# Performance work log

Hardware: AMD Instinct MI355X
Metric: run time of the kernel (lower is better)

## Reference

```python
import jax, jax.numpy as jnp
import numpy as np

D_MODEL = 2048
D_STATE = 16
KER = 4
DT_RANK = D_MODEL // 16  # mamba default: ceil(d_model/16) = 128
B_SZ = 2
SEQ = 1024


def setup_inputs() -> dict:
    key = jax.random.key(0)
    ks = jax.random.split(key, 8)
    s = 0.02
    return {
        "x": jax.random.normal(ks[0], (B_SZ, SEQ, D_MODEL), jnp.float32),
        # in_proj: d_model -> 2*d_inner (expand=1 so d_inner=d_model)
        "W_in": jax.random.normal(ks[1], (2 * D_MODEL, D_MODEL), jnp.float32) * s,
        # depthwise causal conv, one kernel of length KER per channel
        "conv_w": jax.random.normal(ks[2], (D_MODEL, KER), jnp.float32) * s,
        "conv_b": jnp.zeros((D_MODEL,), jnp.float32),
        # x_proj: d_inner -> dt_rank + 2*d_state
        "W_xproj": jax.random.normal(ks[3], (DT_RANK + 2 * D_STATE, D_MODEL), jnp.float32) * s,
        # dt_proj: dt_rank -> d_inner
        "W_dt": jax.random.normal(ks[4], (D_MODEL, DT_RANK), jnp.float32) * s,
        "b_dt": jax.random.uniform(ks[5], (D_MODEL,), jnp.float32, -4.0, -2.0),
        # S4D-real init: A = -[1..d_state] per channel, stored as log
        "A_log": jnp.log(jnp.broadcast_to(jnp.arange(1, D_STATE + 1, dtype=jnp.float32), (D_MODEL, D_STATE))),
        "Dskip": jnp.ones((D_MODEL,), jnp.float32),
        # out_proj: d_inner -> d_model
        "W_out": jax.random.normal(ks[6], (D_MODEL, D_MODEL), jnp.float32) * s,
    }


def _mamba(x, W_in, conv_w, conv_b, W_xproj, W_dt, b_dt, A_log, Dskip, W_out):
    Bsz, L, dm = x.shape
    d_state = A_log.shape[1]
    dt_rank = W_dt.shape[1]
    K = conv_w.shape[1]

    # in_proj -> gate z and ssm input u
    xz = x @ W_in.T                      # [B, L, 2*d_inner]
    u, z = jnp.split(xz, 2, axis=-1)     # each [B, L, d_inner]

    # causal depthwise conv1d over time, then SiLU
    up = jnp.pad(u, ((0, 0), (K - 1, 0), (0, 0)))
    conv = conv_b + sum(conv_w[:, k] * up[:, k:k + L, :] for k in range(K))
    u = jax.nn.silu(conv)                # [B, L, d_inner]

    # input-dependent dt, B, C
    x_dbl = u @ W_xproj.T                # [B, L, dt_rank + 2*d_state]
    dt_r = x_dbl[..., :dt_rank]
    Bm = x_dbl[..., dt_rank:dt_rank + d_state]      # [B, L, N]
    Cm = x_dbl[..., dt_rank + d_state:]             # [B, L, N]
    dt = jax.nn.softplus(dt_r @ W_dt.T + b_dt)      # [B, L, d_inner]

    A = -jnp.exp(A_log)                             # [d_inner, N]
    dA = jnp.exp(dt[..., None] * A)                 # [B, L, d_inner, N]
    dBu = dt[..., None] * Bm[:, :, None, :] * u[..., None]  # [B, L, d_inner, N]

    def step(h, inp):
        dA_t, dBu_t, C_t = inp
        h = dA_t * h + dBu_t                        # [B, d_inner, N]
        y_t = jnp.einsum('bdn,bn->bd', h, C_t)      # [B, d_inner]
        return h, y_t

    h0 = jnp.zeros((Bsz, dm, d_state), dtype=x.dtype)
    _, ys = jax.lax.scan(step, h0,
                         (dA.swapaxes(0, 1), dBu.swapaxes(0, 1), Cm.swapaxes(0, 1)))
    y = ys.swapaxes(0, 1) + u * Dskip               # [B, L, d_inner]
    y = y * jax.nn.silu(z)
    return y @ W_out.T                              # [B, L, d_model]


def reference(x, W_in, conv_w, conv_b, W_xproj, W_dt, b_dt, A_log, Dskip, W_out):
    return _mamba(x, W_in, conv_w, conv_b, W_xproj, W_dt, b_dt, A_log, Dskip, W_out)
```

## Files before the change

### kernel.cpp

```cpp
#include <hip/hip_runtime.h>
#include <hip/hip_bf16.h>


#define D_MODEL 2048
#define D_STATE 16
#define KER 4
#define DT_RANK 128
#define B_SZ 2
#define SEQ 1024
#define BL (B_SZ * SEQ)
#define XPROJ_N (DT_RANK + 2 * D_STATE)
#define NC 32
#define TC (SEQ / NC)

using f32x4  = __attribute__((ext_vector_type(4))) float;
using bf16x8 = __attribute__((ext_vector_type(8))) __bf16;
using bf16x4 = __attribute__((ext_vector_type(4))) __bf16;

__device__ __forceinline__ float softplusf(float x) {
    return (x > 20.f) ? x : log1pf(__expf(x));
}
__device__ __forceinline__ float siluf(float x) {
    return x / (1.f + __expf(-x));
}

__device__ __forceinline__ void split4(const float* __restrict__ src,
                                       __bf16* __restrict__ hi,
                                       __bf16* __restrict__ lo, int i) {
    float4 v = *reinterpret_cast<const float4*>(&src[(size_t)i * 4]);
    bf16x4 hv, lv;
    float f[4] = {v.x, v.y, v.z, v.w};
    #pragma unroll
    for (int j = 0; j < 4; ++j) {
        __bf16 h = (__bf16)f[j];
        hv[j] = h;
        lv[j] = (__bf16)(f[j] - (float)h);
    }
    *reinterpret_cast<bf16x4*>(&hi[(size_t)i * 4]) = hv;
    *reinterpret_cast<bf16x4*>(&lo[(size_t)i * 4]) = lv;
}

__global__ __launch_bounds__(256) void split_all_kernel(
    const float* __restrict__ x,  __bf16* __restrict__ xh,  __bf16* __restrict__ xl,
    const float* __restrict__ wi, __bf16* __restrict__ wih, __bf16* __restrict__ wil,
    const float* __restrict__ wo, __bf16* __restrict__ woh, __bf16* __restrict__ wol,
    const float* __restrict__ wd, __bf16* __restrict__ wdh, __bf16* __restrict__ wdl)
{
    const int NX = BL * D_MODEL / 4;
    const int NI = 2 * D_MODEL * D_MODEL / 4;
    const int NO = D_MODEL * D_MODEL / 4;
    const int ND = D_MODEL * DT_RANK / 4;
    const int total = NX + NI + NO + ND;
    for (int i = blockIdx.x * 256 + threadIdx.x; i < total; i += gridDim.x * 256) {
        if      (i < NX)           split4(x,  xh,  xl,  i);
        else if (i < NX + NI)      split4(wi, wih, wil, i - NX);
        else if (i < NX + NI + NO) split4(wo, woh, wol, i - NX - NI);
        else                       split4(wd, wdh, wdl, i - NX - NI - NO);
    }
}

template <int EPI>
__global__ __launch_bounds__(256, 2) void gemm_bf3(
    const __bf16* __restrict__ Ah, const __bf16* __restrict__ Al,
    const __bf16* __restrict__ Wh, const __bf16* __restrict__ Wl,
    float* __restrict__ C, const float* __restrict__ bias, int N_, int K)
{
    __shared__ __align__(16) __bf16 lds[4 * 128 * 64];
    __bf16* sAh = lds;
    __bf16* sAl = lds + 8192;
    __bf16* sWh = lds + 16384;
    __bf16* sWl = lds + 24576;

    const int tid = threadIdx.x;
    const int bm = blockIdx.y * 128;
    const int bn = blockIdx.x * 128;
    const int w  = tid >> 6;
    const int l  = tid & 63;
    const int wr = (w >> 1) * 64;
    const int wc = (w & 1) * 64;
    const int fr = l & 15;
    const int fq = l >> 4;

    f32x4 acc[4][4] = {};

    for (int k0 = 0; k0 < K; k0 += 64) {
        #pragma unroll
        for (int i = 0; i < 4; ++i) {
            const int f  = i * 256 + tid;
            const int r  = f >> 3;
            const int ss = f & 7;
            const int gs = ss ^ (r & 7);
            const size_t ga = (size_t)(bm + r) * K + k0 + gs * 8;
            const size_t gw = (size_t)(bn + r) * K + k0 + gs * 8;
            __builtin_amdgcn_global_load_lds(
                (const __attribute__((address_space(1))) void*)(Ah + ga),
                (__attribute__((address_space(3))) void*)(sAh + (size_t)f * 8), 16, 0, 0);
            __builtin_amdgcn_global_load_lds(
                (const __attribute__((address_space(1))) void*)(Al + ga),
                (__attribute__((address_space(3))) void*)(sAl + (size_t)f * 8), 16, 0, 0);
            __builtin_amdgcn_global_load_lds(
                (const __attribute__((address_space(1))) void*)(Wh + gw),
                (__attribute__((address_space(3))) void*)(sWh + (size_t)f * 8), 16, 0, 0);
            __builtin_amdgcn_global_load_lds(
                (const __attribute__((address_space(1))) void*)(Wl + gw),
                (__attribute__((address_space(3))) void*)(sWl + (size_t)f * 8), 16, 0, 0);
        }
        __syncthreads();

        #pragma unroll
        for (int ks = 0; ks < 2; ++ks) {
            bf16x8 ah[4], al[4], wh[4], wl[4];
            #pragma unroll
            for (int t = 0; t < 4; ++t) {
                const int ra = wr + t * 16 + fr;
                const int sa = (ks * 4 + fq) ^ (ra & 7);
                ah[t] = *reinterpret_cast<const bf16x8*>(&sAh[ra * 64 + sa * 8]);
                al[t] = *reinterpret_cast<const bf16x8*>(&sAl[ra * 64 + sa * 8]);
                const int rw = wc + t * 16 + fr;
                const int sw = (ks * 4 + fq) ^ (rw & 7);
                wh[t] = *reinterpret_cast<const bf16x8*>(&sWh[rw * 64 + sw * 8]);
                wl[t] = *reinterpret_cast<const bf16x8*>(&sWl[rw * 64 + sw * 8]);
            }
            #pragma unroll
            for (int mt = 0; mt < 4; ++mt)
                #pragma unroll
                for (int nt = 0; nt < 4; ++nt) {
                    acc[mt][nt] = __builtin_amdgcn_mfma_f32_16x16x32_bf16(
                        ah[mt], wh[nt], acc[mt][nt], 0, 0, 0);
                    acc[mt][nt] = __builtin_amdgcn_mfma_f32_16x16x32_bf16(
                        ah[mt], wl[nt], acc[mt][nt], 0, 0, 0);
                    acc[mt][nt] = __builtin_amdgcn_mfma_f32_16x16x32_bf16(
                        al[mt], wh[nt], acc[mt][nt], 0, 0, 0);
                }
        }
        __syncthreads();
    }

    #pragma unroll
    for (int mt = 0; mt < 4; ++mt)
        #pragma unroll
        for (int nt = 0; nt < 4; ++nt) {
            const int gn = bn + wc + nt * 16 + fr;
            #pragma unroll
            for (int j = 0; j < 4; ++j) {
                float v = acc[mt][nt][j];
                if (EPI == 1) v = softplusf(v + bias[gn]);
                C[(size_t)(bm + wr + mt * 16 + fq * 4 + j) * N_ + gn] = v;
            }
        }
}

#define BKT 32
#define XBM 64
#define XBN 32
#define XKS 8
#define XKC (D_MODEL / XKS)

__global__ __launch_bounds__(256) void xdbl_partial(
    const float* __restrict__ A,
    const float* __restrict__ W,
    float* __restrict__ P)
{
    __shared__ float As[BKT][XBM + 4];
    __shared__ float Ws[BKT][XBN + 4];

    const int tid = threadIdx.x;
    const int bm = blockIdx.y * XBM;
    const int bn = blockIdx.x * XBN;
    const int ks = blockIdx.z;
    const int tx = tid & 7;
    const int ty = tid >> 3;

    float acc[2][4] = {};

    const int kend = (ks + 1) * XKC;
    for (int k0 = ks * XKC; k0 < kend; k0 += BKT) {
        #pragma unroll
        for (int i = 0; i < 2; ++i) {
            int f = tid + i * 256;
            int row = f >> 3;
            int kq  = f & 7;
            float4 v = *reinterpret_cast<const float4*>(
                &A[(size_t)(bm + row) * D_MODEL + k0 + kq * 4]);
            As[kq * 4 + 0][row] = v.x;
            As[kq * 4 + 1][row] = v.y;
            As[kq * 4 + 2][row] = v.z;
            As[kq * 4 + 3][row] = v.w;
        }
        {
            int row = tid >> 3;
            int kq  = tid & 7;
            float4 v = *reinterpret_cast<const float4*>(
                &W[(size_t)(bn + row) * D_MODEL + k0 + kq * 4]);
            Ws[kq * 4 + 0][row] = v.x;
            Ws[kq * 4 + 1][row] = v.y;
            Ws[kq * 4 + 2][row] = v.z;
            Ws[kq * 4 + 3][row] = v.w;
        }
        __syncthreads();

        #pragma unroll
        for (int kk = 0; kk < BKT; ++kk) {
            float a0 = As[kk][ty * 2 + 0];
            float a1 = As[kk][ty * 2 + 1];
            float4 w4 = *reinterpret_cast<const float4*>(&Ws[kk][tx * 4]);
            float wv[4] = {w4.x, w4.y, w4.z, w4.w};
            #pragma unroll
            for (int j = 0; j < 4; ++j) {
                acc[0][j] = fmaf(a0, wv[j], acc[0][j]);
                acc[1][j] = fmaf(a1, wv[j], acc[1][j]);
            }
        }
        __syncthreads();
    }

    #pragma unroll
    for (int i = 0; i < 2; ++i) {
        const int gm = bm + ty * 2 + i;
        #pragma unroll
        for (int j = 0; j < 4; ++j) {
            const int gn = bn + tx * 4 + j;
            P[((size_t)ks * BL + gm) * XPROJ_N + gn] = acc[i][j];
        }
    }
}

__global__ __launch_bounds__(256) void xdbl_reduce(
    const float* __restrict__ P, float* __restrict__ xdbl,
    __bf16* __restrict__ xdh, __bf16* __restrict__ xdl)
{
    const int i = blockIdx.x * 256 + threadIdx.x;
    const int n4 = BL * XPROJ_N / 4;
    if (i >= n4) return;
    float4 s = *reinterpret_cast<const float4*>(&P[(size_t)i * 4]);
    #pragma unroll
    for (int ks = 1; ks < XKS; ++ks) {
        float4 v = *reinterpret_cast<const float4*>(
            &P[(size_t)ks * BL * XPROJ_N + (size_t)i * 4]);
        s.x += v.x; s.y += v.y; s.z += v.z; s.w += v.w;
    }
    *reinterpret_cast<float4*>(&xdbl[(size_t)i * 4]) = s;

    const int row = i / (XPROJ_N / 4);
    const int col = (i % (XPROJ_N / 4)) * 4;
    if (col < DT_RANK) {
        bf16x4 hv, lv;
        float f[4] = {s.x, s.y, s.z, s.w};
        #pragma unroll
        for (int j = 0; j < 4; ++j) {
            __bf16 h = (__bf16)f[j];
            hv[j] = h;
            lv[j] = (__bf16)(f[j] - (float)h);
        }
        *reinterpret_cast<bf16x4*>(&xdh[(size_t)row * DT_RANK + col]) = hv;
        *reinterpret_cast<bf16x4*>(&xdl[(size_t)row * DT_RANK + col]) = lv;
    }
}

__global__ __launch_bounds__(256) void conv_silu_kernel(
    const float* __restrict__ xz,
    const float* __restrict__ conv_w,
    const float* __restrict__ conv_b,
    float* __restrict__ u)
{
    int idx = blockIdx.x * 256 + threadIdx.x;
    if (idx >= BL * (D_MODEL / 4)) return;
    const int d4 = (idx & (D_MODEL / 4 - 1)) * 4;
    const int bl = idx >> 9;
    const int l  = bl & (SEQ - 1);
    const int b  = bl >> 10;

    float4 cb = *reinterpret_cast<const float4*>(&conv_b[d4]);
    float4 cw[4];
    #pragma unroll
    for (int j = 0; j < 4; ++j)
        cw[j] = *reinterpret_cast<const float4*>(&conv_w[(d4 + j) * KER]);

    float acc[4] = {cb.x, cb.y, cb.z, cb.w};
    #pragma unroll
    for (int k = 0; k < KER; ++k) {
        const int ls = l - (KER - 1) + k;
        if (ls >= 0) {
            float4 v = *reinterpret_cast<const float4*>(
                &xz[(size_t)(b * SEQ + ls) * (2 * D_MODEL) + d4]);
            acc[0] = fmaf((&cw[0].x)[k], v.x, acc[0]);
            acc[1] = fmaf((&cw[1].x)[k], v.y, acc[1]);
            acc[2] = fmaf((&cw[2].x)[k], v.z, acc[2]);
            acc[3] = fmaf((&cw[3].x)[k], v.w, acc[3]);
        }
    }
    float4 o;
    o.x = siluf(acc[0]); o.y = siluf(acc[1]);
    o.z = siluf(acc[2]); o.w = siluf(acc[3]);
    *reinterpret_cast<float4*>(&u[(size_t)bl * D_MODEL + d4]) = o;
}

__global__ __launch_bounds__(256) void scan_part1(
    const float* __restrict__ dt,
    const float* __restrict__ xdbl,
    const float* __restrict__ u,
    const float* __restrict__ A_log,
    float* __restrict__ PH,
    float* __restrict__ Hend)
{
    const int tid = threadIdx.x;
    const int d   = blockIdx.x * 256 + tid;
    const int bc  = blockIdx.y;
    const int b   = bc >> 5;
    const int c   = bc & (NC - 1);

    float A[16];
    #pragma unroll
    for (int q = 0; q < 4; ++q) {
        float4 v = *reinterpret_cast<const float4*>(&A_log[d * 16 + q * 4]);
        A[q*4+0] = -__expf(v.x); A[q*4+1] = -__expf(v.y);
        A[q*4+2] = -__expf(v.z); A[q*4+3] = -__expf(v.w);
    }
    float h[16] = {};
    float P[16];
    #pragma unroll
    for (int n = 0; n < 16; ++n) P[n] = 1.f;

    const size_t row0 = (size_t)b * SEQ + c * TC;
    for (int t = 0; t < TC; ++t) {
        const size_t row = row0 + t;
        const float dtv = dt[row * D_MODEL + d];
        const float uv  = u[row * D_MODEL + d];
        float Bv[16];
        const float4* Bp = reinterpret_cast<const float4*>(&xdbl[row * XPROJ_N + DT_RANK]);
        #pragma unroll
        for (int q = 0; q < 4; ++q) {
            float4 v = Bp[q];
            Bv[q*4+0] = v.x; Bv[q*4+1] = v.y; Bv[q*4+2] = v.z; Bv[q*4+3] = v.w;
        }
        const float dtu = dtv * uv;
        #pragma unroll
        for (int n = 0; n < 16; ++n) {
            float dA = __expf(dtv * A[n]);
            h[n] = fmaf(dA, h[n], dtu * Bv[n]);
            P[n] *= dA;
        }
    }
    const size_t off = ((size_t)bc * D_MODEL + d) * 16;
    #pragma unroll
    for (int q = 0; q < 4; ++q) {
        *reinterpret_cast<float4*>(&PH[off + q*4])   =
            make_float4(P[q*4+0], P[q*4+1], P[q*4+2], P[q*4+3]);
        *reinterpret_cast<float4*>(&Hend[off + q*4]) =
            make_float4(h[q*4+0], h[q*4+1], h[q*4+2], h[q*4+3]);
    }
}

__global__ __launch_bounds__(256) void scan_part2(
    float* __restrict__ PH,
    const float* __restrict__ Hend)
{
    const int g  = blockIdx.x * 256 + threadIdx.x;
    const int b  = g >> 15;
    const int dn = g & 32767;
    float h = 0.f;
    #pragma unroll
    for (int c = 0; c < NC; ++c) {
        const size_t off = ((size_t)(b * NC + c) * D_MODEL * 16) + dn;
        const float p  = PH[off];
        const float he = Hend[off];
        PH[off] = h;
        h = fmaf(p, h, he);
    }
}

__global__ __launch_bounds__(256) void scan_part3(
    const float* __restrict__ dt,
    const float* __restrict__ xdbl,
    const float* __restrict__ xz,
    const float* __restrict__ u,
    const float* __restrict__ A_log,
    const float* __restrict__ Dskip,
    const float* __restrict__ PH,
    __bf16* __restrict__ yh, __bf16* __restrict__ yl)
{
    const int tid = threadIdx.x;
    const int d   = blockIdx.x * 256 + tid;
    const int bc  = blockIdx.y;
    const int b   = bc >> 5;
    const int c   = bc & (NC - 1);

    float A[16];
    #pragma unroll
    for (int q = 0; q < 4; ++q) {
        float4 v = *reinterpret_cast<const float4*>(&A_log[d * 16 + q * 4]);
        A[q*4+0] = -__expf(v.x); A[q*4+1] = -__expf(v.y);
        A[q*4+2] = -__expf(v.z); A[q*4+3] = -__expf(v.w);
    }
    float h[16];
    const size_t off = ((size_t)bc * D_MODEL + d) * 16;
    #pragma unroll
    for (int q = 0; q < 4; ++q) {
        float4 v = *reinterpret_cast<const float4*>(&PH[off + q*4]);
        h[q*4+0] = v.x; h[q*4+1] = v.y; h[q*4+2] = v.z; h[q*4+3] = v.w;
    }
    const float Dk = Dskip[d];

    const size_t row0 = (size_t)b * SEQ + c * TC;
    for (int t = 0; t < TC; ++t) {
        const size_t row = row0 + t;
        const float dtv = dt[row * D_MODEL + d];
        const float uv  = u[row * D_MODEL + d];
        float Bv[16], Cv[16];
        const float4* Bp = reinterpret_cast<const float4*>(&xdbl[row * XPROJ_N + DT_RANK]);
        const float4* Cp = reinterpret_cast<const float4*>(&xdbl[row * XPROJ_N + DT_RANK + D_STATE]);
        #pragma unroll
        for (int q = 0; q < 4; ++q) {
            float4 v = Bp[q];
            Bv[q*4+0] = v.x; Bv[q*4+1] = v.y; Bv[q*4+2] = v.z; Bv[q*4+3] = v.w;
            float4 wv = Cp[q];
            Cv[q*4+0] = wv.x; Cv[q*4+1] = wv.y; Cv[q*4+2] = wv.z; Cv[q*4+3] = wv.w;
        }
        const float dtu = dtv * uv;
        float y = 0.f;
        #pragma unroll
        for (int n = 0; n < 16; ++n) {
            float dA = __expf(dtv * A[n]);
            h[n] = fmaf(dA, h[n], dtu * Bv[n]);
            y = fmaf(h[n], Cv[n], y);
        }
        const float zv = xz[row * (2 * D_MODEL) + D_MODEL + d];
        const float yv = (y + uv * Dk) * siluf(zv);
        const __bf16 hv = (__bf16)yv;
        yh[row * D_MODEL + d] = hv;
        yl[row * D_MODEL + d] = (__bf16)(yv - (float)hv);
    }
}

extern "C" void kernel_launch(void* const* d_in, const int* in_sizes, int n_in,
                              void* d_out, int out_size, void* d_ws, size_t ws_size,
                              hipStream_t stream) {
    const float* x       = (const float*)d_in[0];
    const float* W_in    = (const float*)d_in[1];
    const float* conv_w  = (const float*)d_in[2];
    const float* conv_b  = (const float*)d_in[3];
    const float* W_xproj = (const float*)d_in[4];
    const float* W_dt    = (const float*)d_in[5];
    const float* b_dt    = (const float*)d_in[6];
    const float* A_log   = (const float*)d_in[7];
    const float* Dskip   = (const float*)d_in[8];
    const float* W_out   = (const float*)d_in[9];
    float* out = (float*)d_out;

    float* ws = (float*)d_ws;
    const size_t M1 = 1024 * 1024;
    float* xz   = ws;
    float* u    = ws + 8 * M1;
    float* xdbl = ws + 12 * M1;
    float* dt   = ws + 12 * M1 + 512 * 1024;
    float* PH   = dt + 4 * M1;
    float* Hend = PH + 2 * M1;
    __bf16* woh = (__bf16*)(ws + 20 * M1 + 512 * 1024);
    __bf16* wol = woh + 4 * M1;
    __bf16* wdh = wol + 4 * M1;
    __bf16* wdl = wdh + 256 * 1024;
    __bf16* xdh = wdl + 256 * 1024;
    __bf16* xdl = xdh + 256 * 1024;
    __bf16* planes = (__bf16*)(ws + 25 * M1);
    __bf16* xh  = planes;
    __bf16* xl  = xh + 4 * M1;
    __bf16* wih = xl + 4 * M1;
    __bf16* wil = wih + 8 * M1;
    __bf16* yh  = xh;
    __bf16* yl  = xl;
    float* xpart = (float*)planes;

    split_all_kernel<<<2048, 256, 0, stream>>>(x, xh, xl, W_in, wih, wil,
                                               W_out, woh, wol, W_dt, wdh, wdl);

    {
        dim3 grid(2 * D_MODEL / 128, BL / 128);
        gemm_bf3<0><<<grid, 256, 0, stream>>>(xh, xl, wih, wil, xz, nullptr,
                                              2 * D_MODEL, D_MODEL);
    }
    conv_silu_kernel<<<BL * (D_MODEL / 4) / 256, 256, 0, stream>>>(xz, conv_w, conv_b, u);

    {
        dim3 grid(XPROJ_N / XBN, BL / XBM, XKS);
        xdbl_partial<<<grid, 256, 0, stream>>>(u, W_xproj, xpart);
        xdbl_reduce<<<(BL * XPROJ_N / 4 + 255) / 256, 256, 0, stream>>>(
            xpart, xdbl, xdh, xdl);
    }
    {
        dim3 grid(D_MODEL / 128, BL / 128);
        gemm_bf3<1><<<grid, 256, 0, stream>>>(xdh, xdl, wdh, wdl, dt, b_dt,
                                              D_MODEL, DT_RANK);
    }
    {
        dim3 grid(D_MODEL / 256, B_SZ * NC);
        scan_part1<<<grid, 256, 0, stream>>>(dt, xdbl, u, A_log, PH, Hend);
        scan_part2<<<B_SZ * D_MODEL * 16 / 256, 256, 0, stream>>>(PH, Hend);
        scan_part3<<<grid, 256, 0, stream>>>(dt, xdbl, xz, u, A_log, Dskip, PH, yh, yl);
    }
    {
        dim3 grid(D_MODEL / 128, BL / 128);
        gemm_bf3<0><<<grid, 256, 0, stream>>>(yh, yl, woh, wol, out, nullptr,
                                              D_MODEL, D_MODEL);
    }
}
```

Baseline: 398.2 us.

## Replace 3-pass bf16 split GEMM with 2-pass scaled fp16 split scheme

Replaces the hi/lo bf16 split GEMM, which needs three MFMAs per tile, with an fp16 scheme. Each operand gets a plain fp16 value plus a second plane storing hi + 512*residual. Two independent accumulators (a1*w1 and a2*w2) are combined in the epilogue as p1 + (p2-p1)/512, which recovers the cross terms. This cuts MFMA work by a third but doubles accumulator registers, and it narrows dynamic range because fp16 can overflow or underflow and the scaled residual adds its own error.

```diff
diff --git a/kernel.cpp b/kernel.cpp
--- a/kernel.cpp
+++ b/kernel.cpp
@@ -12,10 +12,12 @@
 #define XPROJ_N (DT_RANK + 2 * D_STATE)
 #define NC 32
 #define TC (SEQ / NC)
+#define CSCALE 512.0f
+#define CINV (1.0f / 512.0f)
 
 using f32x4  = __attribute__((ext_vector_type(4))) float;
-using bf16x8 = __attribute__((ext_vector_type(8))) __bf16;
-using bf16x4 = __attribute__((ext_vector_type(4))) __bf16;
+using f16x8  = __attribute__((ext_vector_type(8))) _Float16;
+using f16x4  = __attribute__((ext_vector_type(4))) _Float16;
 
 __device__ __forceinline__ float softplusf(float x) {
     return (x > 20.f) ? x : log1pf(__expf(x));
@@ -25,26 +27,27 @@
 }
 
 __device__ __forceinline__ void split4(const float* __restrict__ src,
-                                       __bf16* __restrict__ hi,
-                                       __bf16* __restrict__ lo, int i) {
+                                       _Float16* __restrict__ p1,
+                                       _Float16* __restrict__ p2, int i) {
     float4 v = *reinterpret_cast<const float4*>(&src[(size_t)i * 4]);
-    bf16x4 hv, lv;
+    f16x4 h1, h2;
     float f[4] = {v.x, v.y, v.z, v.w};
     #pragma unroll
     for (int j = 0; j < 4; ++j) {
-        __bf16 h = (__bf16)f[j];
-        hv[j] = h;
-        lv[j] = (__bf16)(f[j] - (float)h);
-    }
-    *reinterpret_cast<bf16x4*>(&hi[(size_t)i * 4]) = hv;
-    *reinterpret_cast<bf16x4*>(&lo[(size_t)i * 4]) = lv;
+        _Float16 h = (_Float16)f[j];
+        float hf = (float)h;
+        h1[j] = h;
+        h2[j] = (_Float16)(fmaf(CSCALE, f[j] - hf, hf));
+    }
+    *reinterpret_cast<f16x4*>(&p1[(size_t)i * 4]) = h1;
+    *reinterpret_cast<f16x4*>(&p2[(size_t)i * 4]) = h2;
 }
 
 __global__ __launch_bounds__(256) void split_all_kernel(
-    const float* __restrict__ x,  __bf16* __restrict__ xh,  __bf16* __restrict__ xl,
-    const float* __restrict__ wi, __bf16* __restrict__ wih, __bf16* __restrict__ wil,
-    const float* __restrict__ wo, __bf16* __restrict__ woh, __bf16* __restrict__ wol,
-    const float* __restrict__ wd, __bf16* __restrict__ wdh, __bf16* __restrict__ wdl)
+    const float* __restrict__ x,  _Float16* __restrict__ x1,  _Float16* __restrict__ x2,
+    const float* __restrict__ wi, _Float16* __restrict__ wi1, _Float16* __restrict__ wi2,
+    const float* __restrict__ wo, _Float16* __restrict__ wo1, _Float16* __restrict__ wo2,
+    const float* __restrict__ wd, _Float16* __restrict__ wd1, _Float16* __restrict__ wd2)
 {
     const int NX = BL * D_MODEL / 4;
     const int NI = 2 * D_MODEL * D_MODEL / 4;
@@ -52,24 +55,24 @@
     const int ND = D_MODEL * DT_RANK / 4;
     const int total = NX + NI + NO + ND;
     for (int i = blockIdx.x * 256 + threadIdx.x; i < total; i += gridDim.x * 256) {
-        if      (i < NX)           split4(x,  xh,  xl,  i);
-        else if (i < NX + NI)      split4(wi, wih, wil, i - NX);
-        else if (i < NX + NI + NO) split4(wo, woh, wol, i - NX - NI);
-        else                       split4(wd, wdh, wdl, i - NX - NI - NO);
+        if      (i < NX)           split4(x,  x1,  x2,  i);
+        else if (i < NX + NI)      split4(wi, wi1, wi2, i - NX);
+        else if (i < NX + NI + NO) split4(wo, wo1, wo2, i - NX - NI);
+        else                       split4(wd, wd1, wd2, i - NX - NI - NO);
     }
 }
 
 template <int EPI>
-__global__ __launch_bounds__(256, 2) void gemm_bf3(
-    const __bf16* __restrict__ Ah, const __bf16* __restrict__ Al,
-    const __bf16* __restrict__ Wh, const __bf16* __restrict__ Wl,
+__global__ __launch_bounds__(256, 2) void gemm_f16c(
+    const _Float16* __restrict__ A1, const _Float16* __restrict__ A2,
+    const _Float16* __restrict__ W1, const _Float16* __restrict__ W2,
     float* __restrict__ C, const float* __restrict__ bias, int N_, int K)
 {
-    __shared__ __align__(16) __bf16 lds[4 * 128 * 64];
-    __bf16* sAh = lds;
-    __bf16* sAl = lds + 8192;
-    __bf16* sWh = lds + 16384;
-    __bf16* sWl = lds + 24576;
+    __shared__ __align__(16) _Float16 lds[4 * 128 * 64];
+    _Float16* sA1 = lds;
+    _Float16* sA2 = lds + 8192;
+    _Float16* sW1 = lds + 16384;
+    _Float16* sW2 = lds + 24576;
 
     const int tid = threadIdx.x;
     const int bm = blockIdx.y * 128;
@@ -81,7 +84,8 @@
     const int fr = l & 15;
     const int fq = l >> 4;
 
-    f32x4 acc[4][4] = {};
+    f32x4 acc1[4][4] = {};
+    f32x4 acc2[4][4] = {};
 
     for (int k0 = 0; k0 < K; k0 += 64) {
         #pragma unroll
@@ -93,44 +97,42 @@
             const size_t ga = (size_t)(bm + r) * K + k0 + gs * 8;
             const size_t gw = (size_t)(bn + r) * K + k0 + gs * 8;
             __builtin_amdgcn_global_load_lds(
-                (const __attribute__((address_space(1))) void*)(Ah + ga),
-                (__attribute__((address_space(3))) void*)(sAh + (size_t)f * 8), 16, 0, 0);
+                (const __attribute__((address_space(1))) void*)(A1 + ga),
+                (__attribute__((address_space(3))) void*)(sA1 + (size_t)f * 8), 16, 0, 0);
             __builtin_amdgcn_global_load_lds(
-                (const __attribute__((address_space(1))) void*)(Al + ga),
-                (__attribute__((address_space(3))) void*)(sAl + (size_t)f * 8), 16, 0, 0);
+                (const __attribute__((address_space(1))) void*)(A2 + ga),
+                (__attribute__((address_space(3))) void*)(sA2 + (size_t)f * 8), 16, 0, 0);
             __builtin_amdgcn_global_load_lds(
-                (const __attribute__((address_space(1))) void*)(Wh + gw),
-                (__attribute__((address_space(3))) void*)(sWh + (size_t)f * 8), 16, 0, 0);
+                (const __attribute__((address_space(1))) void*)(W1 + gw),
+                (__attribute__((address_space(3))) void*)(sW1 + (size_t)f * 8), 16, 0, 0);
             __builtin_amdgcn_global_load_lds(
-                (const __attribute__((address_space(1))) void*)(Wl + gw),
-                (__attribute__((address_space(3))) void*)(sWl + (size_t)f * 8), 16, 0, 0);
+                (const __attribute__((address_space(1))) void*)(W2 + gw),
+                (__attribute__((address_space(3))) void*)(sW2 + (size_t)f * 8), 16, 0, 0);
         }
         __syncthreads();
 
         #pragma unroll
         for (int ks = 0; ks < 2; ++ks) {
-            bf16x8 ah[4], al[4], wh[4], wl[4];
+            f16x8 a1[4], a2[4], w1[4], w2[4];
             #pragma unroll
             for (int t = 0; t < 4; ++t) {
                 const int ra = wr + t * 16 + fr;
                 const int sa = (ks * 4 + fq) ^ (ra & 7);
-                ah[t] = *reinterpret_cast<const bf16x8*>(&sAh[ra * 64 + sa * 8]);
-                al[t] = *reinterpret_cast<const bf16x8*>(&sAl[ra * 64 + sa * 8]);
+                a1[t] = *reinterpret_cast<const f16x8*>(&sA1[ra * 64 + sa * 8]);
+                a2[t] = *reinterpret_cast<const f16x8*>(&sA2[ra * 64 + sa * 8]);
                 const int rw = wc + t * 16 + fr;
                 const int sw = (ks * 4 + fq) ^ (rw & 7);
-                wh[t] = *reinterpret_cast<const bf16x8*>(&sWh[rw * 64 + sw * 8]);
-                wl[t] = *reinterpret_cast<const bf16x8*>(&sWl[rw * 64 + sw * 8]);
+                w1[t] = *reinterpret_cast<const f16x8*>(&sW1[rw * 64 + sw * 8]);
+                w2[t] = *reinterpret_cast<const f16x8*>(&sW2[rw * 64 + sw * 8]);
             }
             #pragma unroll
             for (int mt = 0; mt < 4; ++mt)
                 #pragma unroll
                 for (int nt = 0; nt < 4; ++nt) {
-                    acc[mt][nt] = __builtin_amdgcn_mfma_f32_16x16x32_bf16(
-                        ah[mt], wh[nt], acc[mt][nt], 0, 0, 0);
-                    acc[mt][nt] = __builtin_amdgcn_mfma_f32_16x16x32_bf16(
-                        ah[mt], wl[nt], acc[mt][nt], 0, 0, 0);
-                    acc[mt][nt] = __builtin_amdgcn_mfma_f32_16x16x32_bf16(
-                        al[mt], wh[nt], acc[mt][nt], 0, 0, 0);
+                    acc1[mt][nt] = __builtin_amdgcn_mfma_f32_16x16x32_f16(
+                        a1[mt], w1[nt], acc1[mt][nt], 0, 0, 0);
+                    acc2[mt][nt] = __builtin_amdgcn_mfma_f32_16x16x32_f16(
+                        a2[mt], w2[nt], acc2[mt][nt], 0, 0, 0);
                 }
         }
         __syncthreads();
@@ -143,7 +145,9 @@
             const int gn = bn + wc + nt * 16 + fr;
             #pragma unroll
             for (int j = 0; j < 4; ++j) {
-                float v = acc[mt][nt][j];
+                const float p1 = acc1[mt][nt][j];
+                const float p2 = acc2[mt][nt][j];
+                float v = fmaf(p2 - p1, CINV, p1);
                 if (EPI == 1) v = softplusf(v + bias[gn]);
                 C[(size_t)(bm + wr + mt * 16 + fq * 4 + j) * N_ + gn] = v;
             }
@@ -227,7 +231,7 @@
 
 __global__ __launch_bounds__(256) void xdbl_reduce(
     const float* __restrict__ P, float* __restrict__ xdbl,
-    __bf16* __restrict__ xdh, __bf16* __restrict__ xdl)
+    _Float16* __restrict__ xd1, _Float16* __restrict__ xd2)
 {
     const int i = blockIdx.x * 256 + threadIdx.x;
     const int n4 = BL * XPROJ_N / 4;
@@ -244,16 +248,17 @@
     const int row = i / (XPROJ_N / 4);
     const int col = (i % (XPROJ_N / 4)) * 4;
     if (col < DT_RANK) {
-        bf16x4 hv, lv;
+        f16x4 h1, h2;
         float f[4] = {s.x, s.y, s.z, s.w};
         #pragma unroll
         for (int j = 0; j < 4; ++j) {
-            __bf16 h = (__bf16)f[j];
-            hv[j] = h;
-            lv[j] = (__bf16)(f[j] - (float)h);
-        }
-        *reinterpret_cast<bf16x4*>(&xdh[(size_t)row * DT_RANK + col]) = hv;
-        *reinterpret_cast<bf16x4*>(&xdl[(size_t)row * DT_RANK + col]) = lv;
+            _Float16 h = (_Float16)f[j];
+            float hf = (float)h;
+            h1[j] = h;
+            h2[j] = (_Float16)(fmaf(CSCALE, f[j] - hf, hf));
+        }
+        *reinterpret_cast<f16x4*>(&xd1[(size_t)row * DT_RANK + col]) = h1;
+        *reinterpret_cast<f16x4*>(&xd2[(size_t)row * DT_RANK + col]) = h2;
     }
 }
 
@@ -377,7 +382,7 @@
     const float* __restrict__ A_log,
     const float* __restrict__ Dskip,
     const float* __restrict__ PH,
-    __bf16* __restrict__ yh, __bf16* __restrict__ yl)
+    _Float16* __restrict__ y1, _Float16* __restrict__ y2)
 {
     const int tid = threadIdx.x;
     const int d   = blockIdx.x * 256 + tid;
@@ -426,9 +431,10 @@
         }
         const float zv = xz[row * (2 * D_MODEL) + D_MODEL + d];
         const float yv = (y + uv * Dk) * siluf(zv);
-        const __bf16 hv = (__bf16)yv;
-        yh[row * D_MODEL + d] = hv;
-        yl[row * D_MODEL + d] = (__bf16)(yv - (float)hv);
+        const _Float16 hv = (_Float16)yv;
+        const float hf = (float)hv;
+        y1[row * D_MODEL + d] = hv;
+        y2[row * D_MODEL + d] = (_Float16)(fmaf(CSCALE, yv - hf, hf));
     }
 }
 
@@ -455,28 +461,28 @@
     float* dt   = ws + 12 * M1 + 512 * 1024;
     float* PH   = dt + 4 * M1;
     float* Hend = PH + 2 * M1;
-    __bf16* woh = (__bf16*)(ws + 20 * M1 + 512 * 1024);
-    __bf16* wol = woh + 4 * M1;
-    __bf16* wdh = wol + 4 * M1;
-    __bf16* wdl = wdh + 256 * 1024;
-    __bf16* xdh = wdl + 256 * 1024;
-    __bf16* xdl = xdh + 256 * 1024;
-    __bf16* planes = (__bf16*)(ws + 25 * M1);
-    __bf16* xh  = planes;
-    __bf16* xl  = xh + 4 * M1;
-    __bf16* wih = xl + 4 * M1;
-    __bf16* wil = wih + 8 * M1;
-    __bf16* yh  = xh;
-    __bf16* yl  = xl;
+    _Float16* wo1 = (_Float16*)(ws + 20 * M1 + 512 * 1024);
+    _Float16* wo2 = wo1 + 4 * M1;
+    _Float16* wd1 = wo2 + 4 * M1;
+    _Float16* wd2 = wd1 + 256 * 1024;
+    _Float16* xd1 = wd2 + 256 * 1024;
+    _Float16* xd2 = xd1 + 256 * 1024;
+    _Float16* planes = (_Float16*)(ws + 25 * M1);
+    _Float16* x1  = planes;
+    _Float16* x2  = x1 + 4 * M1;
+    _Float16* wi1 = x2 + 4 * M1;
+    _Float16* wi2 = wi1 + 8 * M1;
+    _Float16* y1 = x1;
+    _Float16* y2 = x2;
     float* xpart = (float*)planes;
 
-    split_all_kernel<<<2048, 256, 0, stream>>>(x, xh, xl, W_in, wih, wil,
-                                               W_out, woh, wol, W_dt, wdh, wdl);
+    split_all_kernel<<<2048, 256, 0, stream>>>(x, x1, x2, W_in, wi1, wi2,
+                                               W_out, wo1, wo2, W_dt, wd1, wd2);
 
     {
         dim3 grid(2 * D_MODEL / 128, BL / 128);
-        gemm_bf3<0><<<grid, 256, 0, stream>>>(xh, xl, wih, wil, xz, nullptr,
-                                              2 * D_MODEL, D_MODEL);
+        gemm_f16c<0><<<grid, 256, 0, stream>>>(x1, x2, wi1, wi2, xz, nullptr,
+                                               2 * D_MODEL, D_MODEL);
     }
     conv_silu_kernel<<<BL * (D_MODEL / 4) / 256, 256, 0, stream>>>(xz, conv_w, conv_b, u);
 
@@ -484,22 +490,22 @@
         dim3 grid(XPROJ_N / XBN, BL / XBM, XKS);
         xdbl_partial<<<grid, 256, 0, stream>>>(u, W_xproj, xpart);
         xdbl_reduce<<<(BL * XPROJ_N / 4 + 255) / 256, 256, 0, stream>>>(
-            xpart, xdbl, xdh, xdl);
+            xpart, xdbl, xd1, xd2);
     }
     {
         dim3 grid(D_MODEL / 128, BL / 128);
-        gemm_bf3<1><<<grid, 256, 0, stream>>>(xdh, xdl, wdh, wdl, dt, b_dt,
-                                              D_MODEL, DT_RANK);
+        gemm_f16c<1><<<grid, 256, 0, stream>>>(xd1, xd2, wd1, wd2, dt, b_dt,
+                                               D_MODEL, DT_RANK);
     }
     {
         dim3 grid(D_MODEL / 256, B_SZ * NC);
         scan_part1<<<grid, 256, 0, stream>>>(dt, xdbl, u, A_log, PH, Hend);
         scan_part2<<<B_SZ * D_MODEL * 16 / 256, 256, 0, stream>>>(PH, Hend);
-        scan_part3<<<grid, 256, 0, stream>>>(dt, xdbl, xz, u, A_log, Dskip, PH, yh, yl);
+        scan_part3<<<grid, 256, 0, stream>>>(dt, xdbl, xz, u, A_log, Dskip, PH, y1, y2);
     }
     {
         dim3 grid(D_MODEL / 128, BL / 128);
-        gemm_bf3<0><<<grid, 256, 0, stream>>>(yh, yl, woh, wol, out, nullptr,
-                                              D_MODEL, D_MODEL);
-    }
-}
+        gemm_f16c<0><<<grid, 256, 0, stream>>>(y1, y2, wo1, wo2, out, nullptr,
+                                               D_MODEL, D_MODEL);
+    }
+}
```

After: 384.1 us. 1.04x faster.
